# Performance work log

Hardware: AMD Instinct MI355X
Metric: run time of the kernel (lower is better)

The kernel has to match this reference:

```python
import jax, jax.numpy as jnp
import numpy as np
from jax import lax

NUM_KP = 17
MAX_PEOPLE = 30
HEAT_THRESH = 0.1
STRIDE = 4  # heatmap -> image coordinate scale

def setup_inputs() -> dict:
    key = jax.random.key(0)
    heatmaps = jax.random.uniform(key, (32, NUM_KP, 256, 256), dtype=jnp.float32)
    return {"heatmaps": heatmaps}

def reference(heatmaps):
    # heatmaps: [B, C, H, W]
    B, C, H, W = heatmaps.shape
    neg_inf = jnp.float32(-jnp.inf)
    # 3x3 max-pool NMS (stride 1, pad 1) batched over all B*C channels at once.
    hmax = lax.reduce_window(
        heatmaps, neg_inf, lax.max,
        window_dimensions=(1, 1, 3, 3),
        window_strides=(1, 1, 1, 1),
        padding=((0, 0), (0, 0), (1, 1), (1, 1)),
    )
    nms = heatmaps * (hmax == heatmaps).astype(heatmaps.dtype)
    # Threshold + descending sort + take top max_people, done as a batched top_k.
    flat = nms.reshape(B, C, H * W)
    masked = jnp.where(flat > HEAT_THRESH, flat, neg_inf)
    scores, idx = lax.top_k(masked, MAX_PEOPLE)          # [B, C, max_people]
    y = idx // W
    x = idx % W
    coords = jnp.stack([x, y], axis=-1).astype(jnp.int32) * STRIDE  # [B,C,max_people,2] as (x,y)*4
    valid = scores > HEAT_THRESH                          # padding mask (original output is ragged)
    return coords, scores, valid
```

## Files before the change

kernel.cpp:

```cpp
#include <hip/hip_runtime.h>
#include <stdint.h>

#define NUM_KP 17
#define BATCH  32
#define HDIM   256
#define WDIM   256
#define NCH    (BATCH * NUM_KP)
#define MAXP   30
#define QBLKS  4
#define K1THREADS 256
#define SEGCAP 640

#define NBINS  4096
#define QB     125953

#define WS_REQUIRED ((size_t)NCH * QBLKS * MAXP * 8)

__device__ __forceinline__ unsigned long long shfl_down_u64(unsigned long long v, int off) {
    unsigned lo = (unsigned)v, hi = (unsigned)(v >> 32);
    lo = __shfl_down(lo, off);
    hi = __shfl_down(hi, off);
    return ((unsigned long long)hi << 32) | lo;
}
__device__ __forceinline__ unsigned long long shfl_u64(unsigned long long v, int lane) {
    unsigned lo = (unsigned)v, hi = (unsigned)(v >> 32);
    lo = __shfl(lo, lane);
    hi = __shfl(hi, lane);
    return ((unsigned long long)hi << 32) | lo;
}
__device__ __forceinline__ unsigned quant12(float v) {
    int b = (int)(__float_as_uint(v) >> 13) - QB;
    b = b < 1 ? 1 : (b > NBINS - 1 ? NBINS - 1 : b);
    return (unsigned)b;
}

__global__ __launch_bounds__(K1THREADS, 7)
void pose_part_kernel(const float* __restrict__ heat, unsigned long long* __restrict__ part) {
    __shared__ unsigned s_buf[4 * SEGCAP];
    __shared__ unsigned s_hist[NBINS / 2];
    __shared__ int s_gsum[256];
    __shared__ unsigned long long s_ref[256];
    __shared__ int s_wcnt[4];
    __shared__ int s_nref, s_tau;

    const int tid  = threadIdx.x;
    const int chan = blockIdx.x >> 2;
    const int qtr  = blockIdx.x & 3;
    const int wave = tid >> 6;
    const int lane = tid & 63;
    const float NEGINF = -__builtin_inff();
    const float* __restrict__ cp = heat + (size_t)chan * (HDIM * WDIM);

    for (int i = tid; i < NBINS / 2; i += K1THREADS) s_hist[i] = 0;
    if (tid == 0) s_nref = 0;
    __syncthreads();

    const int r0 = (qtr << 6) + (wave << 4);
    const float* colp = cp + (lane << 2);
    const float4 NEG4 = make_float4(NEGINF, NEGINF, NEGINF, NEGINF);
    const unsigned long long ltmask = (1ull << lane) - 1ull;
    unsigned* __restrict__ seg = s_buf + wave * SEGCAP;
    int wavecnt = 0;

    auto LD = [&](int r) -> float4 {
        return (r >= 0 && r < HDIM) ? *(const float4*)(colp + (r << 8)) : NEG4;
    };
    auto push = [&](float v, int pidx, int pos) {
        if (pos < SEGCAP) {
            unsigned q = quant12(v);
            seg[pos] = (q << 16) | (unsigned)pidx;
            atomicAdd(&s_hist[q >> 1], 1u << ((q & 1) << 4));
        }
    };
    auto process = [&](const float4& up, const float4& md, const float4& dn, int r) {
        float vm0 = fmaxf(up.x, fmaxf(md.x, dn.x));
        float vm1 = fmaxf(up.y, fmaxf(md.y, dn.y));
        float vm2 = fmaxf(up.z, fmaxf(md.z, dn.z));
        float vm3 = fmaxf(up.w, fmaxf(md.w, dn.w));
        float left  = __shfl_up(vm3, 1);   if (lane == 0)  left  = NEGINF;
        float right = __shfl_down(vm0, 1); if (lane == 63) right = NEGINF;
        float h0 = fmaxf(left, fmaxf(vm0, vm1));
        float h1 = fmaxf(vm0, fmaxf(vm1, vm2));
        float h2 = fmaxf(vm1, fmaxf(vm2, vm3));
        float h3 = fmaxf(vm2, fmaxf(vm3, right));

        bool p0 = md.x > 0.1f && md.x == h0;
        bool p1 = md.y > 0.1f && md.y == h1;
        bool p2 = md.z > 0.1f && md.z == h2;
        bool p3 = md.w > 0.1f && md.w == h3;
        unsigned long long b0 = __ballot(p0), b1 = __ballot(p1);
        unsigned long long b2 = __ballot(p2), b3 = __ballot(p3);
        int c0 = __popcll(b0), c1 = __popcll(b1), c2 = __popcll(b2);
        int before = wavecnt;
        wavecnt += c0 + c1 + c2 + __popcll(b3);

        const int base = (r << 8) | (lane << 2);
        if (p0) push(md.x, base + 0, before + __popcll(b0 & ltmask));
        if (p1) push(md.y, base + 1, before + c0 + __popcll(b1 & ltmask));
        if (p2) push(md.z, base + 2, before + c0 + c1 + __popcll(b2 & ltmask));
        if (p3) push(md.w, base + 3, before + c0 + c1 + c2 + __popcll(b3 & ltmask));
    };

    float4 rm   = LD(r0 - 1);
    float4 cur0 = LD(r0 + 0), cur1 = LD(r0 + 1), cur2 = LD(r0 + 2), cur3 = LD(r0 + 3);
    #pragma unroll
    for (int g = 0; g < 4; ++g) {
        const int rb = r0 + (g << 2);
        float4 n0, n1, n2, n3;
        if (g < 3) { n0 = LD(rb + 4); n1 = LD(rb + 5); n2 = LD(rb + 6); n3 = LD(rb + 7); }
        else       { n0 = LD(rb + 4); n1 = NEG4; n2 = NEG4; n3 = NEG4; }
        process(rm,   cur0, cur1, rb + 0);
        process(cur0, cur1, cur2, rb + 1);
        process(cur1, cur2, cur3, rb + 2);
        process(cur2, cur3, n0,   rb + 3);
        rm = cur3; cur0 = n0; cur1 = n1; cur2 = n2; cur3 = n3;
    }
    if (lane == 0) s_wcnt[wave] = wavecnt < SEGCAP ? wavecnt : SEGCAP;
    __syncthreads();

    {
        int s = 0;
        #pragma unroll
        for (int j = 0; j < 8; ++j) {
            unsigned w = s_hist[tid * 8 + j];
            s += (int)(w & 0xFFFFu) + (int)(w >> 16);
        }
        s_gsum[tid] = s;
    }
    __syncthreads();
    if (wave == 0) {
        int u0 = s_gsum[(lane << 2) + 0], u1 = s_gsum[(lane << 2) + 1];
        int u2 = s_gsum[(lane << 2) + 2], u3 = s_gsum[(lane << 2) + 3];
        int t = u0 + u1 + u2 + u3;
        int R = t;
        #pragma unroll
        for (int off = 1; off < 64; off <<= 1) {
            int v = __shfl_down(R, off);
            if (lane + off < 64) R += v;
        }
        int E = R - t;
        int sg3 = u3 + E, sg2 = u2 + sg3, sg1 = u1 + sg2, sg0 = u0 + sg1;
        unsigned long long mask = __ballot(sg0 >= MAXP);
        if (mask == 0ull) {
            if (lane == 0) s_tau = 0;
        } else {
            int hi = 63 - __builtin_clzll(mask);
            if (lane == hi) {
                int k, above;
                if      (sg3 >= MAXP) { k = 3; above = E;   }
                else if (sg2 >= MAXP) { k = 2; above = sg3; }
                else if (sg1 >= MAXP) { k = 1; above = sg2; }
                else                  { k = 0; above = sg1; }
                int g = (lane << 2) + k;
                int cum = above, tau = 0;
                for (int b = (g << 4) + 15; b >= (g << 4); --b) {
                    cum += (int)((s_hist[b >> 1] >> ((b & 1) << 4)) & 0xFFFFu);
                    if (cum >= MAXP) { tau = b; break; }
                }
                s_tau = tau;
            }
        }
    }
    __syncthreads();

    const unsigned tau = (unsigned)s_tau;
    for (int s = 0; s < 4; ++s) {
        const int c = s_wcnt[s];
        const unsigned* sb = s_buf + s * SEGCAP;
        for (int i = tid; i < c; i += K1THREADS) {
            unsigned p = sb[i];
            if ((p >> 16) >= tau) {
                int pos = atomicAdd(&s_nref, 1);
                if (pos < 256) {
                    unsigned idx = p & 0xFFFFu;
                    float sc = cp[idx];
                    s_ref[pos] = ((unsigned long long)__float_as_uint(sc) << 32) | (unsigned)(~idx);
                }
            }
        }
    }
    __syncthreads();
    const int nref = s_nref < 256 ? s_nref : 256;

    if (tid < 64) {
        unsigned long long* pk = part + (size_t)blockIdx.x * MAXP;
        unsigned long long k0 = (tid       < nref) ? s_ref[tid]       : 0ull;
        unsigned long long k1 = (tid + 64  < nref) ? s_ref[tid + 64]  : 0ull;
        unsigned long long k2 = (tid + 128 < nref) ? s_ref[tid + 128] : 0ull;
        unsigned long long k3 = (tid + 192 < nref) ? s_ref[tid + 192] : 0ull;
        for (int r = 0; r < MAXP; ++r) {
            unsigned long long best = k0; int bs = 0;
            if (k1 > best) { best = k1; bs = 1; }
            if (k2 > best) { best = k2; bs = 2; }
            if (k3 > best) { best = k3; bs = 3; }
            unsigned long long key = best;
            int slot = (bs << 6) | tid;
            #pragma unroll
            for (int off = 32; off > 0; off >>= 1) {
                unsigned long long ok = shfl_down_u64(key, off);
                int os = __shfl_down(slot, off);
                if (ok > key) { key = ok; slot = os; }
            }
            key  = shfl_u64(key, 0);
            slot = __shfl(slot, 0);
            if ((slot & 63) == tid) {
                int which = slot >> 6;
                if      (which == 0) k0 = 0ull;
                else if (which == 1) k1 = 0ull;
                else if (which == 2) k2 = 0ull;
                else                 k3 = 0ull;
            }
            if (tid == 0) pk[r] = key;
        }
    }
}

__global__ __launch_bounds__(64)
void pose_merge_kernel(const unsigned long long* __restrict__ part,
                       float* __restrict__ out, int out_size) {
    const int chan = blockIdx.x;
    const int lane = threadIdx.x;
    const float NEGINF = -__builtin_inff();
    const unsigned long long* pk = part + (size_t)chan * (QBLKS * MAXP);

    unsigned long long k0 = pk[lane];
    unsigned long long k1 = (lane + 64 < QBLKS * MAXP) ? pk[lane + 64] : 0ull;

    for (int r = 0; r < MAXP; ++r) {
        unsigned long long best = k0; int bs = 0;
        if (k1 > best) { best = k1; bs = 1; }
        unsigned long long key = best;
        int slot = (bs << 6) | lane;
        #pragma unroll
        for (int off = 32; off > 0; off >>= 1) {
            unsigned long long ok = shfl_down_u64(key, off);
            int os = __shfl_down(slot, off);
            if (ok > key) { key = ok; slot = os; }
        }
        key  = shfl_u64(key, 0);
        slot = __shfl(slot, 0);
        if ((slot & 63) == lane) {
            if ((slot >> 6) == 0) k0 = 0ull; else k1 = 0ull;
        }
        if (lane == 0) {
            float sc, vld; unsigned idx;
            if (key != 0ull) {
                sc  = __uint_as_float((unsigned)(key >> 32));
                idx = (~(unsigned)key) & 0xFFFFu;
                vld = 1.0f;
            } else { sc = NEGINF; idx = 0u; vld = 0.0f; }
            int x = (int)(idx & 255), y = (int)(idx >> 8);
            long long cb = ((long long)chan * MAXP + r) * 2;
            if (cb + 1 < out_size) {
                out[cb]     = (float)(x * 4);
                out[cb + 1] = (float)(y * 4);
            }
            long long so = (long long)NCH * MAXP * 2 + (long long)chan * MAXP + r;
            if (so < out_size) out[so] = sc;
            long long vo = (long long)NCH * MAXP * 3 + (long long)chan * MAXP + r;
            if (vo < out_size) out[vo] = vld;
        }
    }
}

extern "C" void kernel_launch(void* const* d_in, const int* in_sizes, int n_in,
                              void* d_out, int out_size, void* d_ws, size_t ws_size,
                              hipStream_t stream) {
    const float* heat = (const float*)d_in[0];
    float* out = (float*)d_out;
    unsigned long long* part = (unsigned long long*)d_ws;
    hipLaunchKernelGGL(pose_part_kernel, dim3(NCH * QBLKS), dim3(K1THREADS), 0, stream,
                       heat, part);
    hipLaunchKernelGGL(pose_merge_kernel, dim3(NCH), dim3(64), 0, stream,
                       part, out, out_size);
}
```

Before: 236.9 us.

## Fuse merge into part kernel with last-block reduction and rank-based selection

Replaces the serial 30-round wave-shuffle top-k in both stages with a parallel rank-counting selection, where each candidate counts how many keys exceed it. The separate merge kernel is folded into the main kernel: the last of the four blocks per channel, found with an atomic counter and threadfence, merges the partials. This removes a kernel launch and the serial shuffle loops, but adds a memset launch, atomics, and quadratic rank loops over shared memory.

```diff
diff --git a/kernel.cpp b/kernel.cpp
--- a/kernel.cpp
+++ b/kernel.cpp
@@ -13,21 +13,11 @@
 
 #define NBINS  4096
 #define QB     125953
-
-#define WS_REQUIRED ((size_t)NCH * QBLKS * MAXP * 8)
-
-__device__ __forceinline__ unsigned long long shfl_down_u64(unsigned long long v, int off) {
-    unsigned lo = (unsigned)v, hi = (unsigned)(v >> 32);
-    lo = __shfl_down(lo, off);
-    hi = __shfl_down(hi, off);
-    return ((unsigned long long)hi << 32) | lo;
-}
-__device__ __forceinline__ unsigned long long shfl_u64(unsigned long long v, int lane) {
-    unsigned lo = (unsigned)v, hi = (unsigned)(v >> 32);
-    lo = __shfl(lo, lane);
-    hi = __shfl(hi, lane);
-    return ((unsigned long long)hi << 32) | lo;
-}
+#define NPART  (QBLKS * MAXP)
+
+#define PART_BYTES  ((size_t)NCH * QBLKS * MAXP * 8)
+#define WS_REQUIRED (PART_BYTES + (size_t)NCH * 4)
+
 __device__ __forceinline__ unsigned quant12(float v) {
     int b = (int)(__float_as_uint(v) >> 13) - QB;
     b = b < 1 ? 1 : (b > NBINS - 1 ? NBINS - 1 : b);
@@ -35,13 +25,17 @@
 }
 
 __global__ __launch_bounds__(K1THREADS, 7)
-void pose_part_kernel(const float* __restrict__ heat, unsigned long long* __restrict__ part) {
+void pose_fused_kernel(const float* __restrict__ heat,
+                       unsigned long long* __restrict__ part,
+                       int* __restrict__ done_cnt,
+                       float* __restrict__ out, int out_size) {
     __shared__ unsigned s_buf[4 * SEGCAP];
     __shared__ unsigned s_hist[NBINS / 2];
     __shared__ int s_gsum[256];
     __shared__ unsigned long long s_ref[256];
+    __shared__ unsigned long long s_mk[NPART];
     __shared__ int s_wcnt[4];
-    __shared__ int s_nref, s_tau;
+    __shared__ int s_nref, s_tau, s_last, s_nv;
 
     const int tid  = threadIdx.x;
     const int chan = blockIdx.x >> 2;
@@ -182,84 +176,60 @@
     __syncthreads();
     const int nref = s_nref < 256 ? s_nref : 256;
 
-    if (tid < 64) {
-        unsigned long long* pk = part + (size_t)blockIdx.x * MAXP;
-        unsigned long long k0 = (tid       < nref) ? s_ref[tid]       : 0ull;
-        unsigned long long k1 = (tid + 64  < nref) ? s_ref[tid + 64]  : 0ull;
-        unsigned long long k2 = (tid + 128 < nref) ? s_ref[tid + 128] : 0ull;
-        unsigned long long k3 = (tid + 192 < nref) ? s_ref[tid + 192] : 0ull;
-        for (int r = 0; r < MAXP; ++r) {
-            unsigned long long best = k0; int bs = 0;
-            if (k1 > best) { best = k1; bs = 1; }
-            if (k2 > best) { best = k2; bs = 2; }
-            if (k3 > best) { best = k3; bs = 3; }
-            unsigned long long key = best;
-            int slot = (bs << 6) | tid;
-            #pragma unroll
-            for (int off = 32; off > 0; off >>= 1) {
-                unsigned long long ok = shfl_down_u64(key, off);
-                int os = __shfl_down(slot, off);
-                if (ok > key) { key = ok; slot = os; }
-            }
-            key  = shfl_u64(key, 0);
-            slot = __shfl(slot, 0);
-            if ((slot & 63) == tid) {
-                int which = slot >> 6;
-                if      (which == 0) k0 = 0ull;
-                else if (which == 1) k1 = 0ull;
-                else if (which == 2) k2 = 0ull;
-                else                 k3 = 0ull;
-            }
-            if (tid == 0) pk[r] = key;
-        }
-    }
-}
-
-__global__ __launch_bounds__(64)
-void pose_merge_kernel(const unsigned long long* __restrict__ part,
-                       float* __restrict__ out, int out_size) {
-    const int chan = blockIdx.x;
-    const int lane = threadIdx.x;
-    const float NEGINF = -__builtin_inff();
-    const unsigned long long* pk = part + (size_t)chan * (QBLKS * MAXP);
-
-    unsigned long long k0 = pk[lane];
-    unsigned long long k1 = (lane + 64 < QBLKS * MAXP) ? pk[lane + 64] : 0ull;
-
-    for (int r = 0; r < MAXP; ++r) {
-        unsigned long long best = k0; int bs = 0;
-        if (k1 > best) { best = k1; bs = 1; }
-        unsigned long long key = best;
-        int slot = (bs << 6) | lane;
-        #pragma unroll
-        for (int off = 32; off > 0; off >>= 1) {
-            unsigned long long ok = shfl_down_u64(key, off);
-            int os = __shfl_down(slot, off);
-            if (ok > key) { key = ok; slot = os; }
-        }
-        key  = shfl_u64(key, 0);
-        slot = __shfl(slot, 0);
-        if ((slot & 63) == lane) {
-            if ((slot >> 6) == 0) k0 = 0ull; else k1 = 0ull;
-        }
-        if (lane == 0) {
-            float sc, vld; unsigned idx;
-            if (key != 0ull) {
-                sc  = __uint_as_float((unsigned)(key >> 32));
-                idx = (~(unsigned)key) & 0xFFFFu;
-                vld = 1.0f;
-            } else { sc = NEGINF; idx = 0u; vld = 0.0f; }
+    unsigned long long* __restrict__ pk = part + (size_t)blockIdx.x * MAXP;
+    if (tid < MAXP) pk[tid] = 0ull;
+    __syncthreads();
+    if (tid < nref) {
+        unsigned long long k = s_ref[tid];
+        int rank = 0;
+        for (int j = 0; j < nref; ++j) rank += (int)(s_ref[j] > k);
+        if (rank < MAXP) pk[rank] = k;
+    }
+    __syncthreads();
+
+    if (tid == 0) {
+        __threadfence();
+        int prev = atomicAdd(&done_cnt[chan], 1);
+        s_last = (prev == QBLKS - 1);
+    }
+    __syncthreads();
+    if (!s_last) return;
+    __threadfence();
+
+    const unsigned long long* __restrict__ ck = part + (size_t)chan * NPART;
+    if (tid < NPART) s_mk[tid] = ck[tid];
+    if (tid == 0) s_nv = 0;
+    __syncthreads();
+
+    unsigned long long mk = (tid < NPART) ? s_mk[tid] : 0ull;
+    if (mk != 0ull) {
+        atomicAdd(&s_nv, 1);
+        int rank = 0;
+        for (int j = 0; j < NPART; ++j) rank += (int)(s_mk[j] > mk);
+        if (rank < MAXP) {
+            float sc = __uint_as_float((unsigned)(mk >> 32));
+            unsigned idx = (~(unsigned)mk) & 0xFFFFu;
             int x = (int)(idx & 255), y = (int)(idx >> 8);
-            long long cb = ((long long)chan * MAXP + r) * 2;
+            long long cb = ((long long)chan * MAXP + rank) * 2;
             if (cb + 1 < out_size) {
                 out[cb]     = (float)(x * 4);
                 out[cb + 1] = (float)(y * 4);
             }
-            long long so = (long long)NCH * MAXP * 2 + (long long)chan * MAXP + r;
+            long long so = (long long)NCH * MAXP * 2 + (long long)chan * MAXP + rank;
             if (so < out_size) out[so] = sc;
-            long long vo = (long long)NCH * MAXP * 3 + (long long)chan * MAXP + r;
-            if (vo < out_size) out[vo] = vld;
-        }
+            long long vo = (long long)NCH * MAXP * 3 + (long long)chan * MAXP + rank;
+            if (vo < out_size) out[vo] = 1.0f;
+        }
+    }
+    __syncthreads();
+    const int nv = s_nv;
+    if (tid >= nv && tid < MAXP) {
+        long long cb = ((long long)chan * MAXP + tid) * 2;
+        if (cb + 1 < out_size) { out[cb] = 0.0f; out[cb + 1] = 0.0f; }
+        long long so = (long long)NCH * MAXP * 2 + (long long)chan * MAXP + tid;
+        if (so < out_size) out[so] = NEGINF;
+        long long vo = (long long)NCH * MAXP * 3 + (long long)chan * MAXP + tid;
+        if (vo < out_size) out[vo] = 0.0f;
     }
 }
 
@@ -269,8 +239,8 @@
     const float* heat = (const float*)d_in[0];
     float* out = (float*)d_out;
     unsigned long long* part = (unsigned long long*)d_ws;
-    hipLaunchKernelGGL(pose_part_kernel, dim3(NCH * QBLKS), dim3(K1THREADS), 0, stream,
-                       heat, part);
-    hipLaunchKernelGGL(pose_merge_kernel, dim3(NCH), dim3(64), 0, stream,
-                       part, out, out_size);
+    int* cnt = (int*)((char*)d_ws + PART_BYTES);
+    hipMemsetAsync(cnt, 0, NCH * sizeof(int), stream);
+    hipLaunchKernelGGL(pose_fused_kernel, dim3(NCH * QBLKS), dim3(K1THREADS), 0, stream,
+                       heat, part, cnt, out, out_size);
 }
```

Result: slower. 432.5 us (+82.5%).
